# Optimization experiments

Hardware: AMD Instinct MI355X
Metric: run time of the kernel (lower is better)

## Reference

```python
import jax, jax.numpy as jnp
import numpy as np


def setup_inputs() -> dict:
    key = jax.random.key(0)
    k1, k2, k3, k4, k5 = jax.random.split(key, 5)
    B, T, D, U = 64, 8192, 256, 128
    return {
        "target": jax.random.normal(k1, (B, T, D), dtype=jnp.float32),
        "source": jax.random.normal(k2, (B, D), dtype=jnp.float32),
        "W1": jax.random.normal(k3, (D, U), dtype=jnp.float32) * (1.0 / np.sqrt(D)),
        "W2": jax.random.normal(k4, (D, U), dtype=jnp.float32) * (1.0 / np.sqrt(D)),
        "attention_vals": jax.random.normal(k5, (U,), dtype=jnp.float32),
    }


def reference(target, source, W1, W2, attention_vals):
    # target: [B,T,D] -> w2 -> [B,T,U]; source: [B,D] -> w1 -> [B,1,U]
    t = jnp.einsum("btd,du->btu", target, W2)
    s = (source @ W1)[:, None, :]
    additive = jnp.tanh(s + t)                      # [B,T,U]
    scores = jnp.einsum("btu,u->bt", additive, attention_vals)  # [B,T]
    return scores
```

## Files before the change

kernel.cpp:

```cpp
#include <hip/hip_runtime.h>
#include <hip/hip_bf16.h>


#define B_ 64
#define T_ 8192
#define D_ 256
#define U_ 128
#define LDSW 264

typedef __attribute__((ext_vector_type(8))) short bf16x8;
typedef __attribute__((ext_vector_type(4))) float f32x4;

__device__ __forceinline__ short f2bf(float f) {
    unsigned u = __builtin_bit_cast(unsigned, f);
    u += 0x7fffu + ((u >> 16) & 1u);
    return (short)(u >> 16);
}

__device__ __forceinline__ float fast_tanh(float x) {
    float e = __expf(2.0f * x);
    return 1.0f - 2.0f * __builtin_amdgcn_rcpf(e + 1.0f);
}

__device__ __forceinline__ bf16x8 cvt8(const float4& a, const float4& b) {
    union { __hip_bfloat162 h[4]; bf16x8 v; } u;
    u.h[0] = __float22bfloat162_rn(make_float2(a.x, a.y));
    u.h[1] = __float22bfloat162_rn(make_float2(a.z, a.w));
    u.h[2] = __float22bfloat162_rn(make_float2(b.x, b.y));
    u.h[3] = __float22bfloat162_rn(make_float2(b.z, b.w));
    return u.v;
}

__global__ __launch_bounds__(512)
__attribute__((amdgpu_waves_per_eu(4, 4)))
void additive_attn_kernel(
        const float* __restrict__ target,
        const float* __restrict__ source,
        const float* __restrict__ W1,
        const float* __restrict__ W2,
        const float* __restrict__ attn,
        float* __restrict__ out) {
    __shared__ __attribute__((aligned(16))) short lds_w2[U_ * LDSW];
    __shared__ float  lds_red[512];
    __shared__ float2 lds_sa[U_];

    const int tid = threadIdx.x;
    const int bx  = blockIdx.x;
    const int b   = bx >> 3;
    const int tb  = (bx & 7) << 10;

    const int lane = tid & 63;
    const int wave = tid >> 6;
    const int c = lane & 15;
    const int g = lane >> 4;

    const float* tgt  = target + ((size_t)b * T_ + tb) * D_;
    float*       outp = out + (size_t)b * T_ + tb;
    const float* Abase = tgt + (size_t)(wave * 16 + c) * D_ + g * 8;

    float4 p0, p1, p2, p3, q0, q1, q2, q3, r0, r1, r2, r3;

#define LOADB(X0, X1, X2, X3, BI) do {                                        \
    const float* p_ = Abase + (size_t)((BI) >> 2) * (128 * D_) + ((BI) & 3) * 64; \
    X0 = *(const float4*)(p_);      X1 = *(const float4*)(p_ + 4);            \
    X2 = *(const float4*)(p_ + 32); X3 = *(const float4*)(p_ + 36);           \
} while (0)

    LOADB(p0, p1, p2, p3, 0);
    LOADB(q0, q1, q2, q3, 1);

    {
        const int u    = tid & (U_ - 1);
        const int dblk = (tid >> 7) << 6;
        #pragma unroll
        for (int w = 0; w < 8; ++w) {
            const int d0 = dblk + w * 8;
            bf16x8 v;
            #pragma unroll
            for (int i = 0; i < 8; ++i)
                v[i] = f2bf(W2[(size_t)(d0 + i) * U_ + u]);
            *(bf16x8*)&lds_w2[u * LDSW + d0] = v;
        }
    }

    {
        const float* src = source + b * D_;
        const int u    = tid & (U_ - 1);
        const int part = tid >> 7;
        float acc = 0.f;
        #pragma unroll 8
        for (int d = part * 64; d < part * 64 + 64; ++d)
            acc = fmaf(src[d], W1[(size_t)d * U_ + u], acc);
        lds_red[tid] = acc;
    }
    __syncthreads();
    if (tid < U_)
        lds_sa[tid] = make_float2(
            lds_red[tid] + lds_red[tid + 128] + lds_red[tid + 256] + lds_red[tid + 384],
            attn[tid]);
    __syncthreads();

    f32x4 acc[8];
    #pragma unroll
    for (int j = 0; j < 8; ++j) acc[j] = (f32x4){0.f, 0.f, 0.f, 0.f};

#define COMP(X0, X1, X2, X3, Q) do {                                          \
    bf16x8 af0 = cvt8(X0, X1);                                                \
    bf16x8 af1 = cvt8(X2, X3);                                                \
    const int kb_ = (Q) * 64 + g * 8;                                         \
    _Pragma("unroll")                                                         \
    for (int j = 0; j < 8; ++j) {                                             \
        bf16x8 w0 = *(const bf16x8*)&lds_w2[(16 * j + c) * LDSW + kb_];       \
        acc[j] = __builtin_amdgcn_mfma_f32_16x16x32_bf16(w0, af0, acc[j], 0, 0, 0); \
        bf16x8 w1 = *(const bf16x8*)&lds_w2[(16 * j + c) * LDSW + kb_ + 32];  \
        acc[j] = __builtin_amdgcn_mfma_f32_16x16x32_bf16(w1, af1, acc[j], 0, 0, 0); \
    }                                                                         \
} while (0)

#define EPI(IT) do {                                                          \
    float sc = 0.f;                                                           \
    _Pragma("unroll")                                                         \
    for (int j = 0; j < 8; ++j) {                                             \
        float4 sa01 = *(const float4*)&lds_sa[16 * j + 4 * g];                \
        float4 sa23 = *(const float4*)&lds_sa[16 * j + 4 * g + 2];            \
        sc += fast_tanh(acc[j][0] + sa01.x) * sa01.y;                         \
        sc += fast_tanh(acc[j][1] + sa01.z) * sa01.w;                         \
        sc += fast_tanh(acc[j][2] + sa23.x) * sa23.y;                         \
        sc += fast_tanh(acc[j][3] + sa23.z) * sa23.w;                         \
        acc[j] = (f32x4){0.f, 0.f, 0.f, 0.f};                                 \
    }                                                                         \
    sc += __shfl_xor(sc, 16);                                                 \
    sc += __shfl_xor(sc, 32);                                                 \
    if (lane < 16) outp[(IT) * 128 + wave * 16 + lane] = sc;                  \
} while (0)

    #pragma unroll
    for (int bi = 0; bi < 32; ++bi) {
        if (bi % 3 == 0) {
            if (bi < 30) LOADB(r0, r1, r2, r3, bi + 2);
            COMP(p0, p1, p2, p3, bi & 3);
        } else if (bi % 3 == 1) {
            if (bi < 30) LOADB(p0, p1, p2, p3, bi + 2);
            COMP(q0, q1, q2, q3, bi & 3);
        } else {
            if (bi < 30) LOADB(q0, q1, q2, q3, bi + 2);
            COMP(r0, r1, r2, r3, bi & 3);
        }
        if ((bi & 3) == 3) EPI(bi >> 2);
    }

#undef LOADB
#undef COMP
#undef EPI
}

extern "C" void kernel_launch(void* const* d_in, const int* in_sizes, int n_in,
                              void* d_out, int out_size, void* d_ws, size_t ws_size,
                              hipStream_t stream) {
    const float* target = (const float*)d_in[0];
    const float* source = (const float*)d_in[1];
    const float* W1     = (const float*)d_in[2];
    const float* W2     = (const float*)d_in[3];
    const float* attn   = (const float*)d_in[4];
    float* out = (float*)d_out;

    dim3 grid(B_ * (T_ / 1024));
    dim3 block(512);
    hipLaunchKernelGGL(additive_attn_kernel, grid, block, 0, stream,
                       target, source, W1, W2, attn, out);
}
```

Before: 107.9 us.

## Keep W2 fragments in registers and stage target tiles through double-buffered LDS

The kernel now stores the W2 weights as bf16 MFMA fragments in registers, with each wave owning a 32-wide U slice. Target rows are streamed with coalesced loads into a double-buffered bf16 LDS tile of 32 rows. Per-wave partial scores are reduced across the four U-quarters through LDS before the output store. This removes the repeated LDS reads of W2 and the strided per-lane global loads of target. In exchange it adds a block-wide barrier per 32-row tile and an extra LDS write/read round trip for the activations.

```diff
diff --git a/kernel.cpp b/kernel.cpp
--- a/kernel.cpp
+++ b/kernel.cpp
@@ -7,8 +7,11 @@
 #define D_ 256
 #define U_ 128
 #define LDSW 264
+#define TROWS 32
+#define NTILES 32
 
 typedef __attribute__((ext_vector_type(8))) short bf16x8;
+typedef __attribute__((ext_vector_type(4))) short bf16x4;
 typedef __attribute__((ext_vector_type(4))) float f32x4;
 
 __device__ __forceinline__ short f2bf(float f) {
@@ -22,12 +25,10 @@
     return 1.0f - 2.0f * __builtin_amdgcn_rcpf(e + 1.0f);
 }
 
-__device__ __forceinline__ bf16x8 cvt8(const float4& a, const float4& b) {
-    union { __hip_bfloat162 h[4]; bf16x8 v; } u;
+__device__ __forceinline__ bf16x4 cvt4(const float4& a) {
+    union { __hip_bfloat162 h[2]; bf16x4 v; } u;
     u.h[0] = __float22bfloat162_rn(make_float2(a.x, a.y));
     u.h[1] = __float22bfloat162_rn(make_float2(a.z, a.w));
-    u.h[2] = __float22bfloat162_rn(make_float2(b.x, b.y));
-    u.h[3] = __float22bfloat162_rn(make_float2(b.z, b.w));
     return u.v;
 }
 
@@ -40,47 +41,57 @@
         const float* __restrict__ W2,
         const float* __restrict__ attn,
         float* __restrict__ out) {
-    __shared__ __attribute__((aligned(16))) short lds_w2[U_ * LDSW];
+    __shared__ __attribute__((aligned(16))) short lds_tile[2][TROWS * LDSW];
     __shared__ float  lds_red[512];
-    __shared__ float2 lds_sa[U_];
+    __shared__ __attribute__((aligned(16))) float2 lds_sa[U_];
+    __shared__ float  lds_part[2][4][TROWS];
 
-    const int tid = threadIdx.x;
-    const int bx  = blockIdx.x;
-    const int b   = bx >> 3;
-    const int tb  = (bx & 7) << 10;
+    const int tid  = threadIdx.x;
+    const int bx   = blockIdx.x;
+    const int b    = bx >> 3;
+    const int tb   = (bx & 7) << 10;
 
     const int lane = tid & 63;
     const int wave = tid >> 6;
-    const int c = lane & 15;
-    const int g = lane >> 4;
+    const int rg   = wave & 1;
+    const int uq   = wave >> 1;
+    const int c    = lane & 15;
+    const int g    = lane >> 4;
 
     const float* tgt  = target + ((size_t)b * T_ + tb) * D_;
     float*       outp = out + (size_t)b * T_ + tb;
-    const float* Abase = tgt + (size_t)(wave * 16 + c) * D_ + g * 8;
 
-    float4 p0, p1, p2, p3, q0, q1, q2, q3, r0, r1, r2, r3;
+    float4 pl0, pl1, pl2, pl3;
 
-#define LOADB(X0, X1, X2, X3, BI) do {                                        \
-    const float* p_ = Abase + (size_t)((BI) >> 2) * (128 * D_) + ((BI) & 3) * 64; \
-    X0 = *(const float4*)(p_);      X1 = *(const float4*)(p_ + 4);            \
-    X2 = *(const float4*)(p_ + 32); X3 = *(const float4*)(p_ + 36);           \
+#define LOADT(I) do {                                                         \
+    const float* p_ = tgt + (size_t)(I) * (TROWS * D_) + tid * 4;             \
+    pl0 = *(const float4*)(p_);        pl1 = *(const float4*)(p_ + 2048);     \
+    pl2 = *(const float4*)(p_ + 4096); pl3 = *(const float4*)(p_ + 6144);     \
 } while (0)
 
-    LOADB(p0, p1, p2, p3, 0);
-    LOADB(q0, q1, q2, q3, 1);
+#define STORET(BP) do {                                                       \
+    short* d_ = &lds_tile[BP][(tid >> 6) * LDSW + 4 * (tid & 63)];            \
+    *(bf16x4*)(d_ + 0 * 8 * LDSW) = cvt4(pl0);                                \
+    *(bf16x4*)(d_ + 1 * 8 * LDSW) = cvt4(pl1);                                \
+    *(bf16x4*)(d_ + 2 * 8 * LDSW) = cvt4(pl2);                                \
+    *(bf16x4*)(d_ + 3 * 8 * LDSW) = cvt4(pl3);                                \
+} while (0)
 
+    LOADT(0);
+
+    bf16x8 wf[8][2];
     {
-        const int u    = tid & (U_ - 1);
-        const int dblk = (tid >> 7) << 6;
+        const float* wbase = W2 + (size_t)(g * 8) * U_ + uq * 32 + c;
         #pragma unroll
-        for (int w = 0; w < 8; ++w) {
-            const int d0 = dblk + w * 8;
-            bf16x8 v;
+        for (int kk = 0; kk < 8; ++kk)
             #pragma unroll
-            for (int i = 0; i < 8; ++i)
-                v[i] = f2bf(W2[(size_t)(d0 + i) * U_ + u]);
-            *(bf16x8*)&lds_w2[u * LDSW + d0] = v;
-        }
+            for (int j = 0; j < 2; ++j) {
+                const float* wp = wbase + (size_t)(kk * 32) * U_ + 16 * j;
+                bf16x8 v;
+                #pragma unroll
+                for (int e = 0; e < 8; ++e) v[e] = f2bf(wp[(size_t)e * U_]);
+                wf[kk][j] = v;
+            }
     }
 
     {
@@ -98,60 +109,63 @@
         lds_sa[tid] = make_float2(
             lds_red[tid] + lds_red[tid + 128] + lds_red[tid + 256] + lds_red[tid + 384],
             attn[tid]);
+    STORET(0);
+    LOADT(1);
     __syncthreads();
 
-    f32x4 acc[8];
-    #pragma unroll
-    for (int j = 0; j < 8; ++j) acc[j] = (f32x4){0.f, 0.f, 0.f, 0.f};
-
-#define COMP(X0, X1, X2, X3, Q) do {                                          \
-    bf16x8 af0 = cvt8(X0, X1);                                                \
-    bf16x8 af1 = cvt8(X2, X3);                                                \
-    const int kb_ = (Q) * 64 + g * 8;                                         \
-    _Pragma("unroll")                                                         \
-    for (int j = 0; j < 8; ++j) {                                             \
-        bf16x8 w0 = *(const bf16x8*)&lds_w2[(16 * j + c) * LDSW + kb_];       \
-        acc[j] = __builtin_amdgcn_mfma_f32_16x16x32_bf16(w0, af0, acc[j], 0, 0, 0); \
-        bf16x8 w1 = *(const bf16x8*)&lds_w2[(16 * j + c) * LDSW + kb_ + 32];  \
-        acc[j] = __builtin_amdgcn_mfma_f32_16x16x32_bf16(w1, af1, acc[j], 0, 0, 0); \
+#define BODY(I, P) do {                                                       \
+    if ((I) < NTILES - 1) STORET(1 - (P));                                    \
+    if ((I) < NTILES - 2) LOADT((I) + 2);                                     \
+    {                                                                         \
+        const short* trow = &lds_tile[P][(rg * 16 + c) * LDSW + g * 8];       \
+        f32x4 a0 = (f32x4){0.f, 0.f, 0.f, 0.f};                               \
+        f32x4 a1 = (f32x4){0.f, 0.f, 0.f, 0.f};                               \
+        _Pragma("unroll")                                                     \
+        for (int kk = 0; kk < 8; ++kk) {                                      \
+            bf16x8 tf = *(const bf16x8*)(trow + kk * 32);                     \
+            a0 = __builtin_amdgcn_mfma_f32_16x16x32_bf16(wf[kk][0], tf, a0, 0, 0, 0); \
+            a1 = __builtin_amdgcn_mfma_f32_16x16x32_bf16(wf[kk][1], tf, a1, 0, 0, 0); \
+        }                                                                     \
+        float sc = 0.f;                                                       \
+        {                                                                     \
+            const float4 sa01 = *(const float4*)&lds_sa[uq * 32 + 4 * g];     \
+            const float4 sa23 = *(const float4*)&lds_sa[uq * 32 + 4 * g + 2]; \
+            sc += fast_tanh(a0[0] + sa01.x) * sa01.y;                         \
+            sc += fast_tanh(a0[1] + sa01.z) * sa01.w;                         \
+            sc += fast_tanh(a0[2] + sa23.x) * sa23.y;                         \
+            sc += fast_tanh(a0[3] + sa23.z) * sa23.w;                         \
+        }                                                                     \
+        {                                                                     \
+            const float4 sa01 = *(const float4*)&lds_sa[uq * 32 + 16 + 4 * g];\
+            const float4 sa23 = *(const float4*)&lds_sa[uq * 32 + 18 + 4 * g];\
+            sc += fast_tanh(a1[0] + sa01.x) * sa01.y;                         \
+            sc += fast_tanh(a1[1] + sa01.z) * sa01.w;                         \
+            sc += fast_tanh(a1[2] + sa23.x) * sa23.y;                         \
+            sc += fast_tanh(a1[3] + sa23.z) * sa23.w;                         \
+        }                                                                     \
+        sc += __shfl_xor(sc, 16);                                             \
+        sc += __shfl_xor(sc, 32);                                             \
+        if (lane < 16) lds_part[P][uq][rg * 16 + lane] = sc;                  \
     }                                                                         \
+    if ((I) > 0 && tid < TROWS)                                               \
+        outp[((I) - 1) * TROWS + tid] =                                       \
+            lds_part[1 - (P)][0][tid] + lds_part[1 - (P)][1][tid] +           \
+            lds_part[1 - (P)][2][tid] + lds_part[1 - (P)][3][tid];            \
+    __syncthreads();                                                          \
 } while (0)
 
-#define EPI(IT) do {                                                          \
-    float sc = 0.f;                                                           \
-    _Pragma("unroll")                                                         \
-    for (int j = 0; j < 8; ++j) {                                             \
-        float4 sa01 = *(const float4*)&lds_sa[16 * j + 4 * g];                \
-        float4 sa23 = *(const float4*)&lds_sa[16 * j + 4 * g + 2];            \
-        sc += fast_tanh(acc[j][0] + sa01.x) * sa01.y;                         \
-        sc += fast_tanh(acc[j][1] + sa01.z) * sa01.w;                         \
-        sc += fast_tanh(acc[j][2] + sa23.x) * sa23.y;                         \
-        sc += fast_tanh(acc[j][3] + sa23.z) * sa23.w;                         \
-        acc[j] = (f32x4){0.f, 0.f, 0.f, 0.f};                                 \
-    }                                                                         \
-    sc += __shfl_xor(sc, 16);                                                 \
-    sc += __shfl_xor(sc, 32);                                                 \
-    if (lane < 16) outp[(IT) * 128 + wave * 16 + lane] = sc;                  \
-} while (0)
+    for (int ii = 0; ii < NTILES; ii += 2) {
+        BODY(ii, 0);
+        BODY(ii + 1, 1);
+    }
+    if (tid < TROWS)
+        outp[(NTILES - 1) * TROWS + tid] =
+            lds_part[1][0][tid] + lds_part[1][1][tid] +
+            lds_part[1][2][tid] + lds_part[1][3][tid];
 
-    #pragma unroll
-    for (int bi = 0; bi < 32; ++bi) {
-        if (bi % 3 == 0) {
-            if (bi < 30) LOADB(r0, r1, r2, r3, bi + 2);
-            COMP(p0, p1, p2, p3, bi & 3);
-        } else if (bi % 3 == 1) {
-            if (bi < 30) LOADB(p0, p1, p2, p3, bi + 2);
-            COMP(q0, q1, q2, q3, bi & 3);
-        } else {
-            if (bi < 30) LOADB(q0, q1, q2, q3, bi + 2);
-            COMP(r0, r1, r2, r3, bi & 3);
-        }
-        if ((bi & 3) == 3) EPI(bi >> 2);
-    }
-
-#undef LOADB
-#undef COMP
-#undef EPI
+#undef LOADT
+#undef STORET
+#undef BODY
 }
 
 extern "C" void kernel_launch(void* const* d_in, const int* in_sizes, int n_in,
```

New measurement: 172.5 us. 1.6x slower.
